# Kernel tuning notes

Measured on AMD Instinct MI355X. Metric: run time of the kernel, lower is better.

## Reference

```python
import jax, jax.numpy as jnp
import numpy as np
from jax import lax


def setup_inputs() -> dict:
    key = jax.random.key(0)
    k1, k2 = jax.random.split(key)
    L, B, d = 2048, 16, 1024
    x = jax.random.normal(k1, (L, B, d), dtype=jnp.float32)
    val_range = (3.0 / d) ** 0.5
    weight = jax.random.uniform(k2, (d, 3 * d), dtype=jnp.float32,
                                minval=-val_range, maxval=val_range)
    bias = jnp.zeros((2 * d,), dtype=jnp.float32)
    c0 = jnp.zeros((B, d), dtype=jnp.float32)
    return {"x": x, "weight": weight, "bias": bias, "c0": c0}


def reference(x, weight, bias, c0):
    # x: [L, B, d]; weight: [d, 3d]; bias: [2d]; c0: [B, d]
    L, B, d = x.shape
    u = (x.reshape(-1, d) @ weight).reshape(L, B, d, 3)
    x_tilde = u[..., 0]                               # [L, B, d]
    forget = jax.nn.sigmoid(u[..., 1] + bias[:d])     # [L, B, d]
    reset = jax.nn.sigmoid(u[..., 2] + bias[d:])      # [L, B, d]
    # k == 3 case: x_prime is the raw input (highway connection)
    x_prime = x

    def step(c_prev, ft_xt):
        ft, xt = ft_xt
        c = (c_prev - xt) * ft + xt
        return c, c

    c_last, cs = lax.scan(step, c0, (forget, x_tilde))
    g = jnp.tanh(cs)  # activation_type == 1
    h = (g - x_prime) * reset + x_prime
    return h, c_last
```

## Files before the change

### kernel.cpp

```cpp
#include <hip/hip_runtime.h>

#define L_SEQ 2048
#define BATCH 16
#define DDIM  1024
#define MDIM  (L_SEQ * BATCH)
#define NDIM  (3 * DDIM)
#define KDIM  DDIM
#define CH    (BATCH * DDIM)
#define NSEG  32
#define SEGL  64

typedef __attribute__((ext_vector_type(8))) short short8;
typedef __attribute__((ext_vector_type(4))) float f32x4;

static __device__ __forceinline__ unsigned short f2bf(float f) {
  unsigned int u = __builtin_bit_cast(unsigned int, f);
  unsigned int lsb = (u >> 16) & 1u;
  u += 0x7fffu + lsb;
  return (unsigned short)(u >> 16);
}
static __device__ __forceinline__ float bf2f(unsigned short s) {
  unsigned int u = ((unsigned int)s) << 16;
  return __builtin_bit_cast(float, u);
}

static __device__ __forceinline__ void gll16(const void* g, void* l) {
  __builtin_amdgcn_global_load_lds(
      (const __attribute__((address_space(1))) unsigned int*)g,
      (__attribute__((address_space(3))) unsigned int*)l, 16, 0, 0);
}


__global__ void k_convert_x(const float4* __restrict__ x, ushort4* __restrict__ xb, int n4) {
  int i = blockIdx.x * blockDim.x + threadIdx.x;
  int stride = gridDim.x * blockDim.x;
  for (; i < n4; i += stride) {
    float4 v = x[i];
    ushort4 o;
    o.x = f2bf(v.x); o.y = f2bf(v.y); o.z = f2bf(v.z); o.w = f2bf(v.w);
    xb[i] = o;
  }
}

__global__ void k_convert_w(const float* __restrict__ w, unsigned short* __restrict__ wb) {
  int gid = blockIdx.x * 256 + threadIdx.x;
  int k = gid & (KDIM - 1);
  int n = gid >> 10;
  int col = (n < DDIM) ? 3 * n : (n < 2 * DDIM) ? 3 * (n - DDIM) + 1 : 3 * (n - 2 * DDIM) + 2;
  wb[gid] = f2bf(w[(size_t)k * NDIM + col]);
}


#define MFMA1(I, J, A, B) \
  acc[I][J] = __builtin_amdgcn_mfma_f32_16x16x32_bf16(A, B, acc[I][J], 0, 0, 0);

#define MFMAQ(BASE, A0, A1, A2, A3, B0, B1, B2, B3)  \
  MFMA1(BASE + 0, 0, A0, B0) MFMA1(BASE + 0, 1, A0, B1) \
  MFMA1(BASE + 0, 2, A0, B2) MFMA1(BASE + 0, 3, A0, B3) \
  MFMA1(BASE + 1, 0, A1, B0) MFMA1(BASE + 1, 1, A1, B1) \
  MFMA1(BASE + 1, 2, A1, B2) MFMA1(BASE + 1, 3, A1, B3) \
  MFMA1(BASE + 2, 0, A2, B0) MFMA1(BASE + 2, 1, A2, B1) \
  MFMA1(BASE + 2, 2, A2, B2) MFMA1(BASE + 2, 3, A2, B3) \
  MFMA1(BASE + 3, 0, A3, B0) MFMA1(BASE + 3, 1, A3, B1) \
  MFMA1(BASE + 3, 2, A3, B2) MFMA1(BASE + 3, 3, A3, B3)

#define TILE(J, X0, X1, X2, X3, Y0, Y1, Y2, Y3) do {                         \
  const char* Ab  = LDSc + (((J)) & 3) * 32768;                              \
  const char* AbN = LDSc + (((J) + 1) & 3) * 32768;                          \
  char* Sb = LDSc + (((J) + 2) & 3) * 32768;                                 \
  const int kbS = ((i * 4 + (J) + 2) & 31) * 64;                             \
  q0 = *(const short8*)(Ab + aRd + 4096);                                    \
  q1 = *(const short8*)(Ab + aRd + 5120);                                    \
  q2 = *(const short8*)(Ab + aRd + 6144);                                    \
  q3 = *(const short8*)(Ab + aRd + 7168);                                    \
  gll16(srcA0 + kbS, Sb + dstOff);                                           \
  gll16(srcA1 + kbS, Sb + 8192 + dstOff);                                    \
  __builtin_amdgcn_s_setprio(1);                                             \
  MFMAQ(0, p0, p1, p2, p3, X0, X1, X2, X3)                                   \
  __builtin_amdgcn_s_setprio(0);                                             \
  gll16(srcB0 + kbS, Sb + 16384 + dstOff);                                   \
  gll16(srcB1 + kbS, Sb + 24576 + dstOff);                                   \
  __builtin_amdgcn_sched_barrier(0);                                         \
  asm volatile("s_waitcnt vmcnt(4)" ::: "memory");                           \
  __builtin_amdgcn_s_barrier();                                              \
  __builtin_amdgcn_sched_barrier(0);                                         \
  p0 = *(const short8*)(AbN + aRd);                                          \
  p1 = *(const short8*)(AbN + aRd + 1024);                                   \
  p2 = *(const short8*)(AbN + aRd + 2048);                                   \
  p3 = *(const short8*)(AbN + aRd + 3072);                                   \
  Y0 = *(const short8*)(AbN + 16384 + bRd);                                  \
  Y1 = *(const short8*)(AbN + 16384 + bRd + 1024);                           \
  Y2 = *(const short8*)(AbN + 16384 + bRd + 2048);                           \
  Y3 = *(const short8*)(AbN + 16384 + bRd + 3072);                           \
  __builtin_amdgcn_s_setprio(1);                                             \
  MFMAQ(4, q0, q1, q2, q3, X0, X1, X2, X3)                                   \
  __builtin_amdgcn_s_setprio(0);                                             \
} while (0)

__global__ __launch_bounds__(512, 2) void k_gemm256(
    const unsigned short* __restrict__ xb,
    const unsigned short* __restrict__ wb,
    const float* __restrict__ bias,
    unsigned short* __restrict__ xtb,
    unsigned short* __restrict__ fbuf,
    unsigned short* __restrict__ rbuf) {
  __shared__ char LDS[131072];
  char* LDSc = LDS;

  const int tid  = threadIdx.x;
  const int lane = tid & 63;
  const int wid  = tid >> 6;
  const int wr   = wid >> 2;
  const int wc   = wid & 3;

  int bid = blockIdx.x;
  int wg = (bid & 7) * 192 + (bid >> 3);
  int mt = wg / 12;
  int nt = wg - mt * 12;
  const int rowBase = mt * 256;
  const int colBase = nt * 256;

  const int l15 = lane & 15;
  const int sl  = lane >> 4;
  const int ra0 = wr * 128 + l15;
  const int rb0 = wc * 64 + l15;
  const int aRd = ra0 * 64 + (sl ^ ((ra0 >> 1) & 3)) * 16;
  const int bRd = rb0 * 64 + (sl ^ ((rb0 >> 1) & 3)) * 16;

  const int p0i = tid, p1i = 512 + tid;
  const int r0 = p0i >> 2, r1 = p1i >> 2;
  const int s0 = (p0i & 3) ^ ((r0 >> 1) & 3);
  const int s1 = (p1i & 3) ^ ((r1 >> 1) & 3);
  const char* srcA0 = (const char*)xb + (size_t)(rowBase + r0) * 2048 + s0 * 16;
  const char* srcA1 = (const char*)xb + (size_t)(rowBase + r1) * 2048 + s1 * 16;
  const char* srcB0 = (const char*)wb + (size_t)(colBase + r0) * 2048 + s0 * 16;
  const char* srcB1 = (const char*)wb + (size_t)(colBase + r1) * 2048 + s1 * 16;
  const int dstOff = wid * 1024;

  f32x4 acc[8][4];
#pragma unroll
  for (int ii = 0; ii < 8; ++ii)
#pragma unroll
    for (int jj = 0; jj < 4; ++jj)
      acc[ii][jj] = (f32x4){0.f, 0.f, 0.f, 0.f};

#pragma unroll
  for (int u = 0; u < 2; ++u) {
    char* ldsu = LDSc + u * 32768;
    gll16(srcA0 + u * 64, ldsu + dstOff);
    gll16(srcA1 + u * 64, ldsu + 8192 + dstOff);
    gll16(srcB0 + u * 64, ldsu + 16384 + dstOff);
    gll16(srcB1 + u * 64, ldsu + 24576 + dstOff);
  }
  asm volatile("s_waitcnt vmcnt(4)" ::: "memory");
  __builtin_amdgcn_s_barrier();
  __builtin_amdgcn_sched_barrier(0);

  short8 p0, p1, p2, p3;
  short8 q0, q1, q2, q3;
  short8 e0, e1, e2, e3;
  short8 o0, o1, o2, o3;

  p0 = *(const short8*)(LDSc + aRd);
  p1 = *(const short8*)(LDSc + aRd + 1024);
  p2 = *(const short8*)(LDSc + aRd + 2048);
  p3 = *(const short8*)(LDSc + aRd + 3072);
  e0 = *(const short8*)(LDSc + 16384 + bRd);
  e1 = *(const short8*)(LDSc + 16384 + bRd + 1024);
  e2 = *(const short8*)(LDSc + 16384 + bRd + 2048);
  e3 = *(const short8*)(LDSc + 16384 + bRd + 3072);

  for (int i = 0; i < 8; ++i) {
    TILE(0, e0, e1, e2, e3, o0, o1, o2, o3);
    TILE(1, o0, o1, o2, o3, e0, e1, e2, e3);
    TILE(2, e0, e1, e2, e3, o0, o1, o2, o3);
    TILE(3, o0, o1, o2, o3, e0, e1, e2, e3);
  }
  asm volatile("s_waitcnt vmcnt(0)" ::: "memory");

  const int region = colBase >> 10;
#pragma unroll
  for (int qm = 0; qm < 2; ++qm) {
#pragma unroll
    for (int m = 0; m < 4; ++m) {
      int grow = rowBase + wr * 128 + qm * 64 + m * 16 + ((lane >> 4) << 2);
#pragma unroll
      for (int n = 0; n < 4; ++n) {
        int gcol = colBase + wc * 64 + n * 16 + (lane & 15);
        f32x4 v = acc[qm * 4 + m][n];
        if (region == 0) {
#pragma unroll
          for (int j = 0; j < 4; ++j)
            xtb[(size_t)(grow + j) * DDIM + gcol] = f2bf(v[j]);
        } else {
          float bv = bias[gcol - DDIM];
          unsigned short* dst = (region == 1) ? fbuf : rbuf;
          int lcol = gcol - (region << 10);
#pragma unroll
          for (int j = 0; j < 4; ++j) {
            float sg = 1.0f / (1.0f + __expf(-(v[j] + bv)));
            dst[(size_t)(grow + j) * DDIM + lcol] = f2bf(sg);
          }
        }
      }
    }
  }
}


__global__ __launch_bounds__(256) void k_scan1(
    const unsigned short* __restrict__ fbuf,
    const unsigned short* __restrict__ xtb,
    float4* __restrict__ AB) {
  int chp = blockIdx.x * 256 + threadIdx.x;
  int seg = blockIdx.y;
  size_t base = (size_t)seg * SEGL * CH + chp * 2;
  const unsigned int* fp = (const unsigned int*)(fbuf + base);
  const unsigned int* xp = (const unsigned int*)(xtb + base);
  float a0 = 1.f, a1 = 1.f, b0 = 0.f, b1 = 0.f;
#pragma unroll 8
  for (int s = 0; s < SEGL; ++s) {
    unsigned int fv = fp[(size_t)s * (CH / 2)];
    unsigned int xv = xp[(size_t)s * (CH / 2)];
    float f0 = bf2f((unsigned short)fv), f1 = bf2f((unsigned short)(fv >> 16));
    float x0 = bf2f((unsigned short)xv), x1 = bf2f((unsigned short)(xv >> 16));
    b0 = (b0 - x0) * f0 + x0;  a0 *= f0;
    b1 = (b1 - x1) * f1 + x1;  a1 *= f1;
  }
  AB[(size_t)seg * (CH / 2) + chp] = (float4){a0, b0, a1, b1};
}


__global__ __launch_bounds__(256) void k_scan2(
    const float* __restrict__ c0,
    const float4* __restrict__ AB,
    float* __restrict__ Cin,
    float* __restrict__ clast) {
  int chp = blockIdx.x * 256 + threadIdx.x;
  float2 cc = ((const float2*)c0)[chp];
  float ca = cc.x, cb = cc.y;
#pragma unroll
  for (int s = 0; s < NSEG; ++s) {
    ((float2*)Cin)[(size_t)s * (CH / 2) + chp] = (float2){ca, cb};
    float4 ab = AB[(size_t)s * (CH / 2) + chp];
    ca = ca * ab.x + ab.y;
    cb = cb * ab.z + ab.w;
  }
  ((float2*)clast)[chp] = (float2){ca, cb};
}


__global__ __launch_bounds__(256) void k_scan3(
    const float* __restrict__ x,
    const unsigned short* __restrict__ fbuf,
    const unsigned short* __restrict__ xtb,
    const unsigned short* __restrict__ rbuf,
    const float* __restrict__ Cin,
    float* __restrict__ h) {
  int chp = blockIdx.x * 256 + threadIdx.x;
  int seg = blockIdx.y;
  float2 cc = ((const float2*)Cin)[(size_t)seg * (CH / 2) + chp];
  float ca = cc.x, cb = cc.y;
  size_t base = (size_t)seg * SEGL * CH + chp * 2;
  const unsigned int* fp = (const unsigned int*)(fbuf + base);
  const unsigned int* tp = (const unsigned int*)(xtb + base);
  const unsigned int* rp = (const unsigned int*)(rbuf + base);
  const float2* xp = (const float2*)(x + base);
  float2* hp = (float2*)(h + base);
#pragma unroll 4
  for (int s = 0; s < SEGL; ++s) {
    unsigned int fv = fp[(size_t)s * (CH / 2)];
    unsigned int tv = tp[(size_t)s * (CH / 2)];
    unsigned int rv = rp[(size_t)s * (CH / 2)];
    float2 xv = xp[(size_t)s * (CH / 2)];
    float f0 = bf2f((unsigned short)fv), f1 = bf2f((unsigned short)(fv >> 16));
    float t0 = bf2f((unsigned short)tv), t1 = bf2f((unsigned short)(tv >> 16));
    float r0 = bf2f((unsigned short)rv), r1 = bf2f((unsigned short)(rv >> 16));
    ca = (ca - t0) * f0 + t0;
    cb = (cb - t1) * f1 + t1;
    float e0 = __expf(-2.f * fabsf(ca));
    float e1 = __expf(-2.f * fabsf(cb));
    float g0 = copysignf((1.f - e0) / (1.f + e0), ca);
    float g1 = copysignf((1.f - e1) / (1.f + e1), cb);
    float h0 = (g0 - xv.x) * r0 + xv.x;
    float h1 = (g1 - xv.y) * r1 + xv.y;
    hp[(size_t)s * (CH / 2)] = (float2){h0, h1};
  }
}


extern "C" void kernel_launch(void* const* d_in, const int* in_sizes, int n_in,
                              void* d_out, int out_size, void* d_ws, size_t ws_size,
                              hipStream_t stream) {
  const float* x    = (const float*)d_in[0];
  const float* w    = (const float*)d_in[1];
  const float* bias = (const float*)d_in[2];
  const float* c0   = (const float*)d_in[3];
  float* out = (float*)d_out;
  char* ws = (char*)d_ws;

  unsigned short* wb   = (unsigned short*)(ws);
  float4*         AB   = (float4*)(ws);
  float*          Cin  = (float*)(ws + 4194304);
  unsigned short* xtb  = (unsigned short*)(ws + 6291456);
  unsigned short* fbuf = (unsigned short*)(ws + 73400320);
  unsigned short* rbuf = (unsigned short*)(ws + 140509184);
  unsigned short* xb = (unsigned short*)d_out;

  k_convert_x<<<2048, 256, 0, stream>>>((const float4*)x, (ushort4*)xb, MDIM * KDIM / 4);
  k_convert_w<<<(NDIM * KDIM) / 256, 256, 0, stream>>>(w, wb);

  k_gemm256<<<1536, 512, 0, stream>>>(xb, wb, bias, xtb, fbuf, rbuf);

  k_scan1<<<dim3(32, NSEG), 256, 0, stream>>>(fbuf, xtb, AB);
  k_scan2<<<32, 256, 0, stream>>>(c0, AB, Cin, out + (size_t)L_SEQ * CH);
  k_scan3<<<dim3(32, NSEG), 256, 0, stream>>>(x, fbuf, xtb, rbuf, Cin, out);
}
```

Baseline: 409.3 us.

## Restructure GEMM main loop into double-buffered 64-wide K tiles with phase barriers

```diff
diff --git a/kernel.cpp b/kernel.cpp
--- a/kernel.cpp
+++ b/kernel.cpp
@@ -54,47 +54,82 @@
 #define MFMA1(I, J, A, B) \
   acc[I][J] = __builtin_amdgcn_mfma_f32_16x16x32_bf16(A, B, acc[I][J], 0, 0, 0);
 
-#define MFMAQ(BASE, A0, A1, A2, A3, B0, B1, B2, B3)  \
-  MFMA1(BASE + 0, 0, A0, B0) MFMA1(BASE + 0, 1, A0, B1) \
-  MFMA1(BASE + 0, 2, A0, B2) MFMA1(BASE + 0, 3, A0, B3) \
-  MFMA1(BASE + 1, 0, A1, B0) MFMA1(BASE + 1, 1, A1, B1) \
-  MFMA1(BASE + 1, 2, A1, B2) MFMA1(BASE + 1, 3, A1, B3) \
-  MFMA1(BASE + 2, 0, A2, B0) MFMA1(BASE + 2, 1, A2, B1) \
-  MFMA1(BASE + 2, 2, A2, B2) MFMA1(BASE + 2, 3, A2, B3) \
-  MFMA1(BASE + 3, 0, A3, B0) MFMA1(BASE + 3, 1, A3, B1) \
-  MFMA1(BASE + 3, 2, A3, B2) MFMA1(BASE + 3, 3, A3, B3)
-
-#define TILE(J, X0, X1, X2, X3, Y0, Y1, Y2, Y3) do {                         \
-  const char* Ab  = LDSc + (((J)) & 3) * 32768;                              \
-  const char* AbN = LDSc + (((J) + 1) & 3) * 32768;                          \
-  char* Sb = LDSc + (((J) + 2) & 3) * 32768;                                 \
-  const int kbS = ((i * 4 + (J) + 2) & 31) * 64;                             \
-  q0 = *(const short8*)(Ab + aRd + 4096);                                    \
-  q1 = *(const short8*)(Ab + aRd + 5120);                                    \
-  q2 = *(const short8*)(Ab + aRd + 6144);                                    \
-  q3 = *(const short8*)(Ab + aRd + 7168);                                    \
-  gll16(srcA0 + kbS, Sb + dstOff);                                           \
-  gll16(srcA1 + kbS, Sb + 8192 + dstOff);                                    \
-  __builtin_amdgcn_s_setprio(1);                                             \
-  MFMAQ(0, p0, p1, p2, p3, X0, X1, X2, X3)                                   \
-  __builtin_amdgcn_s_setprio(0);                                             \
-  gll16(srcB0 + kbS, Sb + 16384 + dstOff);                                   \
-  gll16(srcB1 + kbS, Sb + 24576 + dstOff);                                   \
-  __builtin_amdgcn_sched_barrier(0);                                         \
-  asm volatile("s_waitcnt vmcnt(4)" ::: "memory");                           \
-  __builtin_amdgcn_s_barrier();                                              \
-  __builtin_amdgcn_sched_barrier(0);                                         \
-  p0 = *(const short8*)(AbN + aRd);                                          \
-  p1 = *(const short8*)(AbN + aRd + 1024);                                   \
-  p2 = *(const short8*)(AbN + aRd + 2048);                                   \
-  p3 = *(const short8*)(AbN + aRd + 3072);                                   \
-  Y0 = *(const short8*)(AbN + 16384 + bRd);                                  \
-  Y1 = *(const short8*)(AbN + 16384 + bRd + 1024);                           \
-  Y2 = *(const short8*)(AbN + 16384 + bRd + 2048);                           \
-  Y3 = *(const short8*)(AbN + 16384 + bRd + 3072);                           \
-  __builtin_amdgcn_s_setprio(1);                                             \
-  MFMAQ(4, q0, q1, q2, q3, X0, X1, X2, X3)                                   \
-  __builtin_amdgcn_s_setprio(0);                                             \
+#define MFMAQ(BASE)                                   \
+  MFMA1(BASE + 0, 0, aa0, bb0) MFMA1(BASE + 0, 1, aa0, bb1) \
+  MFMA1(BASE + 0, 2, aa0, bb2) MFMA1(BASE + 0, 3, aa0, bb3) \
+  MFMA1(BASE + 1, 0, aa1, bb0) MFMA1(BASE + 1, 1, aa1, bb1) \
+  MFMA1(BASE + 1, 2, aa1, bb2) MFMA1(BASE + 1, 3, aa1, bb3) \
+  MFMA1(BASE + 2, 0, aa2, bb0) MFMA1(BASE + 2, 1, aa2, bb1) \
+  MFMA1(BASE + 2, 2, aa2, bb2) MFMA1(BASE + 2, 3, aa2, bb3) \
+  MFMA1(BASE + 3, 0, aa3, bb0) MFMA1(BASE + 3, 1, aa3, bb1) \
+  MFMA1(BASE + 3, 2, aa3, bb2) MFMA1(BASE + 3, 3, aa3, bb3)
+
+#define PH_BAR() do {                           \
+  __builtin_amdgcn_sched_barrier(0);            \
+  __builtin_amdgcn_s_barrier();                 \
+  asm volatile("" ::: "memory");                \
+  __builtin_amdgcn_sched_barrier(0);            \
+} while (0)
+
+#define VM_WAIT4() do {                                   \
+  __builtin_amdgcn_sched_barrier(0);                      \
+  asm volatile("s_waitcnt vmcnt(4)" ::: "memory");        \
+} while (0)
+
+#define TILE64(T) do {                                                        \
+  const char* bufC = LDSc + ((T) & 1) * 65536;                                \
+  char*       bufN = LDSc + (((T) + 1) & 1) * 65536;                          \
+  const int stA = (((T) + 1) & 15) * 128;                                     \
+                 \
+  aa0 = *(const short8*)(bufC + aRd);                                         \
+  aa1 = *(const short8*)(bufC + aRd + 1024);                                  \
+  aa2 = *(const short8*)(bufC + aRd + 2048);                                  \
+  aa3 = *(const short8*)(bufC + aRd + 3072);                                  \
+  bb0 = *(const short8*)(bufC + 32768 + bRd);                                 \
+  bb1 = *(const short8*)(bufC + 32768 + bRd + 1024);                          \
+  bb2 = *(const short8*)(bufC + 32768 + bRd + 2048);                          \
+  bb3 = *(const short8*)(bufC + 32768 + bRd + 3072);                          \
+  gll16(srcA0 + stA, bufN + dstOff);                                          \
+  gll16(srcA1 + stA, bufN + 8192 + dstOff);                                   \
+  PH_BAR();                                                                   \
+  __builtin_amdgcn_s_setprio(1); MFMAQ(0) __builtin_amdgcn_s_setprio(0);      \
+  PH_BAR();                                                                   \
+              \
+  aa0 = *(const short8*)(bufC + aRd + 4096);                                  \
+  aa1 = *(const short8*)(bufC + aRd + 5120);                                  \
+  aa2 = *(const short8*)(bufC + aRd + 6144);                                  \
+  aa3 = *(const short8*)(bufC + aRd + 7168);                                  \
+  gll16(srcB0 + stA, bufN + 32768 + dstOff);                                  \
+  gll16(srcB1 + stA, bufN + 40960 + dstOff);                                  \
+  PH_BAR();                                                                   \
+  __builtin_amdgcn_s_setprio(1); MFMAQ(4) __builtin_amdgcn_s_setprio(0);      \
+  VM_WAIT4();                                                                 \
+  PH_BAR();                                                                   \
+                 \
+  aa0 = *(const short8*)(bufC + 16384 + aRd);                                 \
+  aa1 = *(const short8*)(bufC + 16384 + aRd + 1024);                          \
+  aa2 = *(const short8*)(bufC + 16384 + aRd + 2048);                          \
+  aa3 = *(const short8*)(bufC + 16384 + aRd + 3072);                          \
+  bb0 = *(const short8*)(bufC + 49152 + bRd);                                 \
+  bb1 = *(const short8*)(bufC + 49152 + bRd + 1024);                          \
+  bb2 = *(const short8*)(bufC + 49152 + bRd + 2048);                          \
+  bb3 = *(const short8*)(bufC + 49152 + bRd + 3072);                          \
+  gll16(srcA0 + stA + 64, bufN + 16384 + dstOff);                             \
+  gll16(srcA1 + stA + 64, bufN + 24576 + dstOff);                             \
+  PH_BAR();                                                                   \
+  __builtin_amdgcn_s_setprio(1); MFMAQ(0) __builtin_amdgcn_s_setprio(0);      \
+  PH_BAR();                                                                   \
+              \
+  aa0 = *(const short8*)(bufC + 16384 + aRd + 4096);                          \
+  aa1 = *(const short8*)(bufC + 16384 + aRd + 5120);                          \
+  aa2 = *(const short8*)(bufC + 16384 + aRd + 6144);                          \
+  aa3 = *(const short8*)(bufC + 16384 + aRd + 7168);                          \
+  gll16(srcB0 + stA + 64, bufN + 49152 + dstOff);                             \
+  gll16(srcB1 + stA + 64, bufN + 57344 + dstOff);                             \
+  PH_BAR();                                                                   \
+  __builtin_amdgcn_s_setprio(1); MFMAQ(4) __builtin_amdgcn_s_setprio(0);      \
+  VM_WAIT4();                                                                 \
+  PH_BAR();                                                                   \
 } while (0)
 
 __global__ __launch_bounds__(512, 2) void k_gemm256(
@@ -144,37 +179,24 @@
     for (int jj = 0; jj < 4; ++jj)
       acc[ii][jj] = (f32x4){0.f, 0.f, 0.f, 0.f};
 
-#pragma unroll
-  for (int u = 0; u < 2; ++u) {
-    char* ldsu = LDSc + u * 32768;
-    gll16(srcA0 + u * 64, ldsu + dstOff);
-    gll16(srcA1 + u * 64, ldsu + 8192 + dstOff);
-    gll16(srcB0 + u * 64, ldsu + 16384 + dstOff);
-    gll16(srcB1 + u * 64, ldsu + 24576 + dstOff);
-  }
-  asm volatile("s_waitcnt vmcnt(4)" ::: "memory");
+  gll16(srcA0, LDSc + dstOff);
+  gll16(srcA1, LDSc + 8192 + dstOff);
+  gll16(srcB0, LDSc + 32768 + dstOff);
+  gll16(srcB1, LDSc + 40960 + dstOff);
+  gll16(srcA0 + 64, LDSc + 16384 + dstOff);
+  gll16(srcA1 + 64, LDSc + 24576 + dstOff);
+  gll16(srcB0 + 64, LDSc + 49152 + dstOff);
+  gll16(srcB1 + 64, LDSc + 57344 + dstOff);
+  asm volatile("s_waitcnt vmcnt(0)" ::: "memory");
   __builtin_amdgcn_s_barrier();
   __builtin_amdgcn_sched_barrier(0);
 
-  short8 p0, p1, p2, p3;
-  short8 q0, q1, q2, q3;
-  short8 e0, e1, e2, e3;
-  short8 o0, o1, o2, o3;
-
-  p0 = *(const short8*)(LDSc + aRd);
-  p1 = *(const short8*)(LDSc + aRd + 1024);
-  p2 = *(const short8*)(LDSc + aRd + 2048);
-  p3 = *(const short8*)(LDSc + aRd + 3072);
-  e0 = *(const short8*)(LDSc + 16384 + bRd);
-  e1 = *(const short8*)(LDSc + 16384 + bRd + 1024);
-  e2 = *(const short8*)(LDSc + 16384 + bRd + 2048);
-  e3 = *(const short8*)(LDSc + 16384 + bRd + 3072);
+  short8 aa0, aa1, aa2, aa3;
+  short8 bb0, bb1, bb2, bb3;
 
   for (int i = 0; i < 8; ++i) {
-    TILE(0, e0, e1, e2, e3, o0, o1, o2, o3);
-    TILE(1, o0, o1, o2, o3, e0, e1, e2, e3);
-    TILE(2, e0, e1, e2, e3, o0, o1, o2, o3);
-    TILE(3, o0, o1, o2, o3, e0, e1, e2, e3);
+    TILE64(2 * i);
+    TILE64(2 * i + 1);
   }
   asm volatile("s_waitcnt vmcnt(0)" ::: "memory");
 
```

Result: no change. 408.6 us (-0.2%).

## Fuse fp32-to-bf16 conversion of x into GEMM A-tile loading

Applied to the files above, without the earlier changes.

```diff
diff --git a/kernel.cpp b/kernel.cpp
--- a/kernel.cpp
+++ b/kernel.cpp
@@ -31,17 +31,6 @@
 }
 
 
-__global__ void k_convert_x(const float4* __restrict__ x, ushort4* __restrict__ xb, int n4) {
-  int i = blockIdx.x * blockDim.x + threadIdx.x;
-  int stride = gridDim.x * blockDim.x;
-  for (; i < n4; i += stride) {
-    float4 v = x[i];
-    ushort4 o;
-    o.x = f2bf(v.x); o.y = f2bf(v.y); o.z = f2bf(v.z); o.w = f2bf(v.w);
-    xb[i] = o;
-  }
-}
-
 __global__ void k_convert_w(const float* __restrict__ w, unsigned short* __restrict__ wb) {
   int gid = blockIdx.x * 256 + threadIdx.x;
   int k = gid & (KDIM - 1);
@@ -64,24 +53,45 @@
   MFMA1(BASE + 3, 0, A3, B0) MFMA1(BASE + 3, 1, A3, B1) \
   MFMA1(BASE + 3, 2, A3, B2) MFMA1(BASE + 3, 3, A3, B3)
 
-#define TILE(J, X0, X1, X2, X3, Y0, Y1, Y2, Y3) do {                         \
+#define CVT_WRITE(W0, W1, W2, W3, DST) do {                                  \
+  short8 _w0, _w1;                                                           \
+  _w0[0] = (short)f2bf(W0.x); _w0[1] = (short)f2bf(W0.y);                    \
+  _w0[2] = (short)f2bf(W0.z); _w0[3] = (short)f2bf(W0.w);                    \
+  _w0[4] = (short)f2bf(W1.x); _w0[5] = (short)f2bf(W1.y);                    \
+  _w0[6] = (short)f2bf(W1.z); _w0[7] = (short)f2bf(W1.w);                    \
+  _w1[0] = (short)f2bf(W2.x); _w1[1] = (short)f2bf(W2.y);                    \
+  _w1[2] = (short)f2bf(W2.z); _w1[3] = (short)f2bf(W2.w);                    \
+  _w1[4] = (short)f2bf(W3.x); _w1[5] = (short)f2bf(W3.y);                    \
+  _w1[6] = (short)f2bf(W3.z); _w1[7] = (short)f2bf(W3.w);                    \
+  *(short8*)((DST) + awr0)        = _w0;                                     \
+  *(short8*)((DST) + 8192 + awr0) = _w1;                                     \
+} while (0)
+
+#define TILE(J, X0, X1, X2, X3, Y0, Y1, Y2, Y3, W0, W1, W2, W3, I0, I1, I2, I3) do { \
   const char* Ab  = LDSc + (((J)) & 3) * 32768;                              \
   const char* AbN = LDSc + (((J) + 1) & 3) * 32768;                          \
   char* Sb = LDSc + (((J) + 2) & 3) * 32768;                                 \
   const int kbS = ((i * 4 + (J) + 2) & 31) * 64;                             \
+  const int kfA = ((i * 4 + (J) + 3) & 31) * 128;                            \
   q0 = *(const short8*)(Ab + aRd + 4096);                                    \
   q1 = *(const short8*)(Ab + aRd + 5120);                                    \
   q2 = *(const short8*)(Ab + aRd + 6144);                                    \
   q3 = *(const short8*)(Ab + aRd + 7168);                                    \
-  gll16(srcA0 + kbS, Sb + dstOff);                                           \
-  gll16(srcA1 + kbS, Sb + 8192 + dstOff);                                    \
+  I0 = *(const float4*)(srcAf0 + kfA);                                       \
+  I1 = *(const float4*)(srcAf0 + kfA + 16);                                  \
+  I2 = *(const float4*)(srcAf1 + kfA);                                       \
+  I3 = *(const float4*)(srcAf1 + kfA + 16);                                  \
+  __builtin_amdgcn_sched_barrier(0);                                         \
+  asm volatile("s_waitcnt vmcnt(6)" ::: "memory");                           \
+  CVT_WRITE(W0, W1, W2, W3, Sb);                                             \
   __builtin_amdgcn_s_setprio(1);                                             \
   MFMAQ(0, p0, p1, p2, p3, X0, X1, X2, X3)                                   \
   __builtin_amdgcn_s_setprio(0);                                             \
   gll16(srcB0 + kbS, Sb + 16384 + dstOff);                                   \
   gll16(srcB1 + kbS, Sb + 24576 + dstOff);                                   \
   __builtin_amdgcn_sched_barrier(0);                                         \
-  asm volatile("s_waitcnt vmcnt(4)" ::: "memory");                           \
+  asm volatile("s_waitcnt vmcnt(6)" ::: "memory");                           \
+  asm volatile("s_waitcnt lgkmcnt(0)" ::: "memory");                         \
   __builtin_amdgcn_s_barrier();                                              \
   __builtin_amdgcn_sched_barrier(0);                                         \
   p0 = *(const short8*)(AbN + aRd);                                          \
@@ -98,7 +108,7 @@
 } while (0)
 
 __global__ __launch_bounds__(512, 2) void k_gemm256(
-    const unsigned short* __restrict__ xb,
+    const float* __restrict__ xf,
     const unsigned short* __restrict__ wb,
     const float* __restrict__ bias,
     unsigned short* __restrict__ xtb,
@@ -131,11 +141,12 @@
   const int r0 = p0i >> 2, r1 = p1i >> 2;
   const int s0 = (p0i & 3) ^ ((r0 >> 1) & 3);
   const int s1 = (p1i & 3) ^ ((r1 >> 1) & 3);
-  const char* srcA0 = (const char*)xb + (size_t)(rowBase + r0) * 2048 + s0 * 16;
-  const char* srcA1 = (const char*)xb + (size_t)(rowBase + r1) * 2048 + s1 * 16;
+  const char* srcAf0 = (const char*)xf + (size_t)(rowBase + r0) * 4096 + s0 * 32;
+  const char* srcAf1 = (const char*)xf + (size_t)(rowBase + r1) * 4096 + s1 * 32;
   const char* srcB0 = (const char*)wb + (size_t)(colBase + r0) * 2048 + s0 * 16;
   const char* srcB1 = (const char*)wb + (size_t)(colBase + r1) * 2048 + s1 * 16;
   const int dstOff = wid * 1024;
+  const int awr0 = tid * 16;
 
   f32x4 acc[8][4];
 #pragma unroll
@@ -144,15 +155,35 @@
     for (int jj = 0; jj < 4; ++jj)
       acc[ii][jj] = (f32x4){0.f, 0.f, 0.f, 0.f};
 
-#pragma unroll
-  for (int u = 0; u < 2; ++u) {
-    char* ldsu = LDSc + u * 32768;
-    gll16(srcA0 + u * 64, ldsu + dstOff);
-    gll16(srcA1 + u * 64, ldsu + 8192 + dstOff);
-    gll16(srcB0 + u * 64, ldsu + 16384 + dstOff);
-    gll16(srcB1 + u * 64, ldsu + 24576 + dstOff);
-  }
-  asm volatile("s_waitcnt vmcnt(4)" ::: "memory");
+  float4 fE0, fE1, fE2, fE3;
+  float4 fO0, fO1, fO2, fO3;
+
+  fE0 = *(const float4*)(srcAf0);
+  fE1 = *(const float4*)(srcAf0 + 16);
+  fE2 = *(const float4*)(srcAf1);
+  fE3 = *(const float4*)(srcAf1 + 16);
+  __builtin_amdgcn_sched_barrier(0);
+  fO0 = *(const float4*)(srcAf0 + 128);
+  fO1 = *(const float4*)(srcAf0 + 144);
+  fO2 = *(const float4*)(srcAf1 + 128);
+  fO3 = *(const float4*)(srcAf1 + 144);
+  __builtin_amdgcn_sched_barrier(0);
+  gll16(srcB0,      LDSc + 16384 + dstOff);
+  gll16(srcB1,      LDSc + 24576 + dstOff);
+  gll16(srcB0 + 64, LDSc + 32768 + 16384 + dstOff);
+  gll16(srcB1 + 64, LDSc + 32768 + 24576 + dstOff);
+  __builtin_amdgcn_sched_barrier(0);
+  CVT_WRITE(fE0, fE1, fE2, fE3, LDSc);
+  __builtin_amdgcn_sched_barrier(0);
+  fE0 = *(const float4*)(srcAf0 + 256);
+  fE1 = *(const float4*)(srcAf0 + 272);
+  fE2 = *(const float4*)(srcAf1 + 256);
+  fE3 = *(const float4*)(srcAf1 + 272);
+  __builtin_amdgcn_sched_barrier(0);
+  CVT_WRITE(fO0, fO1, fO2, fO3, LDSc + 32768);
+  __builtin_amdgcn_sched_barrier(0);
+  asm volatile("s_waitcnt vmcnt(6)" ::: "memory");
+  asm volatile("s_waitcnt lgkmcnt(0)" ::: "memory");
   __builtin_amdgcn_s_barrier();
   __builtin_amdgcn_sched_barrier(0);
 
@@ -171,10 +202,10 @@
   e3 = *(const short8*)(LDSc + 16384 + bRd + 3072);
 
   for (int i = 0; i < 8; ++i) {
-    TILE(0, e0, e1, e2, e3, o0, o1, o2, o3);
-    TILE(1, o0, o1, o2, o3, e0, e1, e2, e3);
-    TILE(2, e0, e1, e2, e3, o0, o1, o2, o3);
-    TILE(3, o0, o1, o2, o3, e0, e1, e2, e3);
+    TILE(0, e0, e1, e2, e3, o0, o1, o2, o3, fE0, fE1, fE2, fE3, fO0, fO1, fO2, fO3);
+    TILE(1, o0, o1, o2, o3, e0, e1, e2, e3, fO0, fO1, fO2, fO3, fE0, fE1, fE2, fE3);
+    TILE(2, e0, e1, e2, e3, o0, o1, o2, o3, fE0, fE1, fE2, fE3, fO0, fO1, fO2, fO3);
+    TILE(3, o0, o1, o2, o3, e0, e1, e2, e3, fO0, fO1, fO2, fO3, fE0, fE1, fE2, fE3);
   }
   asm volatile("s_waitcnt vmcnt(0)" ::: "memory");
 
@@ -305,12 +336,10 @@
   unsigned short* xtb  = (unsigned short*)(ws + 6291456);
   unsigned short* fbuf = (unsigned short*)(ws + 73400320);
   unsigned short* rbuf = (unsigned short*)(ws + 140509184);
-  unsigned short* xb = (unsigned short*)d_out;
-
-  k_convert_x<<<2048, 256, 0, stream>>>((const float4*)x, (ushort4*)xb, MDIM * KDIM / 4);
+
   k_convert_w<<<(NDIM * KDIM) / 256, 256, 0, stream>>>(w, wb);
 
-  k_gemm256<<<1536, 512, 0, stream>>>(xb, wb, bias, xtb, fbuf, rbuf);
+  k_gemm256<<<1536, 512, 0, stream>>>(x, wb, bias, xtb, fbuf, rbuf);
 
   k_scan1<<<dim3(32, NSEG), 256, 0, stream>>>(fbuf, xtb, AB);
   k_scan2<<<32, 256, 0, stream>>>(c0, AB, Cin, out + (size_t)L_SEQ * CH);
```

Result: slower. 682.5 us (+66.8%).
